# Kernel optimization log

Hardware: AMD Instinct MI355X
Metric: run time of the kernel (lower is better)

Reference implementation:

```python
import jax, jax.numpy as jnp
import numpy as np

D_MODEL = 1024
NUM_HEADS = 16
HEAD_DIM = D_MODEL // NUM_HEADS


def setup_inputs() -> dict:
    key = jax.random.key(0)
    ks = jax.random.split(key, 6)
    B, S = 2, 2048
    s = 1.0 / np.sqrt(D_MODEL)
    return {
        "x": jax.random.normal(ks[0], (B, S, D_MODEL), dtype=jnp.float32),
        "Wq": jax.random.normal(ks[1], (D_MODEL, D_MODEL), dtype=jnp.float32) * s,
        "Wk": jax.random.normal(ks[2], (D_MODEL, D_MODEL), dtype=jnp.float32) * s,
        "Wv": jax.random.normal(ks[3], (D_MODEL, D_MODEL), dtype=jnp.float32) * s,
        "Wo": jax.random.normal(ks[4], (D_MODEL, D_MODEL), dtype=jnp.float32) * s,
        "bo": jax.random.normal(ks[5], (D_MODEL,), dtype=jnp.float32) * 0.01,
    }


def reference(x, Wq, Wk, Wv, Wo, bo):
    b, n, _ = x.shape
    # QKV projections (no bias, qkv_bias=False); weights applied as x @ W^T like nn.Linear
    q = (x @ Wq.T).reshape(b, n, NUM_HEADS, HEAD_DIM).transpose(0, 2, 1, 3)  # [b,h,n,d]
    k = (x @ Wk.T).reshape(b, n, NUM_HEADS, HEAD_DIM).transpose(0, 2, 1, 3)
    v = (x @ Wv.T).reshape(b, n, NUM_HEADS, HEAD_DIM).transpose(0, 2, 1, 3)
    scores = jnp.einsum("bhqd,bhkd->bhqk", q, k)
    causal = jnp.tril(jnp.ones((n, n), dtype=bool))  # keep where True
    scores = jnp.where(causal, scores, -jnp.inf)
    weights = jax.nn.softmax(scores / np.sqrt(HEAD_DIM), axis=-1)
    # dropout p=0.0 -> identity (eval semantics)
    ctx = jnp.einsum("bhqk,bhkd->bhqd", weights, v)
    ctx = ctx.transpose(0, 2, 1, 3).reshape(b, n, D_MODEL)
    return ctx @ Wo.T + bo
```

## Files before the change

kernel.cpp:

```cpp
#include <hip/hip_runtime.h>

#define D_MODEL 1024
#define NUM_HEADS 16
#define HEAD_DIM 64
#define BATCH 2
#define SEQ 2048
#define MTOT (BATCH * SEQ)

typedef __attribute__((ext_vector_type(8))) short bf16x8;
typedef __attribute__((ext_vector_type(4))) short s16x4;
typedef __attribute__((ext_vector_type(4))) float f32x4;
typedef unsigned short u16;
typedef unsigned long long u64;

__device__ __forceinline__ u16 f2bf(float f) {
    unsigned u = __float_as_uint(f);
    return (u16)((u + 0x7FFFu + ((u >> 16) & 1u)) >> 16);
}
__device__ __forceinline__ float bf2f(u16 v) {
    return __uint_as_float((unsigned)v << 16);
}

__device__ __forceinline__ unsigned cvt_pk_bf16(float lo, float hi) {
    unsigned r;
    asm volatile("v_cvt_pk_bf16_f32 %0, %1, %2" : "=v"(r) : "v"(lo), "v"(hi));
    return r;
}

#if __has_builtin(__builtin_amdgcn_exp2f)
#define EXP2(x) __builtin_amdgcn_exp2f(x)
#else
#define EXP2(x) exp2f(x)
#endif

#define GLOAD16(gp, lp) __builtin_amdgcn_global_load_lds(                      \
    (const __attribute__((address_space(1))) void*)(gp),                       \
    (__attribute__((address_space(3))) void*)(lp), 16, 0, 0)

__global__ __launch_bounds__(256)
void cast_all_kernel(const float* __restrict__ x,  const float* __restrict__ Wq,
                     const float* __restrict__ Wk, const float* __restrict__ Wv,
                     const float* __restrict__ Wo, u16* __restrict__ dst)
{
    const int i = blockIdx.x * 256 + threadIdx.x;
    const float* src;
    int j;
    if (i < 524288) { src = x; j = i; }
    else if (i < 917504) {
        const int k = i - 524288;
        const int z = k >> 17;
        src = (z == 0) ? Wq : (z == 1) ? Wk : Wv;
        j = k & 0x1FFFF;
    } else { src = Wo; j = i - 917504; }
    const float4* s = reinterpret_cast<const float4*>(src) + (size_t)j * 2;
    float4 a = s[0], b = s[1];
    u16 tmp[8] = {f2bf(a.x), f2bf(a.y), f2bf(a.z), f2bf(a.w),
                  f2bf(b.x), f2bf(b.y), f2bf(b.z), f2bf(b.w)};
    *reinterpret_cast<int4*>(dst + (size_t)i * 8) = *reinterpret_cast<int4*>(tmp);
}

__global__ __launch_bounds__(256)
void gemm_qkv_kernel(const u16* __restrict__ A, const u16* __restrict__ B,
                     u16* __restrict__ Qo, u16* __restrict__ Ko, u16* __restrict__ Vt)
{
    __shared__ u16 Al[128 * 64];
    __shared__ u16 Bl[128 * 64];

    const int tid = threadIdx.x;
    const int l = tid & 63;
    const int w = tid >> 6;
    const int wm = w >> 1, wn = w & 1;
    const int lr = l & 15, lg = l >> 4;
    const int m0 = blockIdx.y * 128;
    const int n0 = blockIdx.x * 128;

    const int srow = tid >> 3;
    const int scol = ((tid & 7) ^ (srow & 7)) * 8;
    const int sxa = (lr & 7) * 8;

    f32x4 acc[4][4];
    #pragma unroll
    for (int i = 0; i < 4; ++i)
        #pragma unroll
        for (int j = 0; j < 4; ++j) acc[i][j] = (f32x4){0.f, 0.f, 0.f, 0.f};

    for (int k0 = 0; k0 < D_MODEL; k0 += 64) {
        __syncthreads();
        #pragma unroll
        for (int i = 0; i < 4; ++i) {
            const u16* ga = A + (size_t)(m0 + i * 32 + srow) * D_MODEL + k0 + scol;
            const u16* gb = B + (size_t)(n0 + i * 32 + srow) * D_MODEL + k0 + scol;
            GLOAD16(ga, Al + i * 2048 + w * 512);
            GLOAD16(gb, Bl + i * 2048 + w * 512);
        }
        __syncthreads();
        #pragma unroll
        for (int kc = 0; kc < 2; ++kc) {
            bf16x8 af[4], bfr[4];
            #pragma unroll
            for (int i = 0; i < 4; ++i)
                af[i] = *reinterpret_cast<const bf16x8*>(
                    &Al[(wm * 64 + i * 16 + lr) * 64 + ((kc * 32 + lg * 8) ^ sxa)]);
            #pragma unroll
            for (int j = 0; j < 4; ++j)
                bfr[j] = *reinterpret_cast<const bf16x8*>(
                    &Bl[(wn * 64 + j * 16 + lr) * 64 + ((kc * 32 + lg * 8) ^ sxa)]);
            #pragma unroll
            for (int i = 0; i < 4; ++i)
                #pragma unroll
                for (int j = 0; j < 4; ++j)
                    acc[i][j] = __builtin_amdgcn_mfma_f32_16x16x32_bf16(
                        af[i], bfr[j], acc[i][j], 0, 0, 0);
        }
    }

    const int z = (n0 >> 10);
    if (z < 2) {
        #pragma unroll
        for (int i = 0; i < 4; ++i) {
            #pragma unroll
            for (int r = 0; r < 4; ++r) {
                const int m = m0 + wm * 64 + i * 16 + lg * 4 + r;
                const int bb = m >> 11, s = m & (SEQ - 1);
                #pragma unroll
                for (int j = 0; j < 4; ++j) {
                    const int c = n0 + wn * 64 + j * 16 + lr;
                    const int cc = c & 1023, h = cc >> 6, d = cc & 63;
                    const size_t idx = ((size_t)(bb * NUM_HEADS + h) * SEQ + s) * 64 + d;
                    if (z == 0) Qo[idx] = f2bf(acc[i][j][r] * 0.18033688f);
                    else        Ko[idx] = f2bf(acc[i][j][r]);
                }
            }
        }
    } else {
        #pragma unroll
        for (int i = 0; i < 4; ++i) {
            const int mbase = m0 + wm * 64 + i * 16 + lg * 4;
            const int bb = mbase >> 11, s = mbase & (SEQ - 1);
            #pragma unroll
            for (int j = 0; j < 4; ++j) {
                const int c = n0 + wn * 64 + j * 16 + lr;
                const int cc = c & 1023, h = cc >> 6, d = cc & 63;
                u16 t4[4];
                #pragma unroll
                for (int r = 0; r < 4; ++r) t4[r] = f2bf(acc[i][j][r]);
                *reinterpret_cast<u64*>(
                    &Vt[((size_t)(bb * NUM_HEADS + h) * 64 + d) * SEQ + s]) =
                    *reinterpret_cast<u64*>(t4);
            }
        }
    }
}

__global__ __launch_bounds__(256)
void gemm_out_kernel(const u16* __restrict__ A, const u16* __restrict__ B,
                     const float* __restrict__ bias, float* __restrict__ out)
{
    __shared__ u16 Al[128 * 64];
    __shared__ u16 Bl[128 * 64];

    const int tid = threadIdx.x;
    const int l = tid & 63;
    const int w = tid >> 6;
    const int wm = w >> 1, wn = w & 1;
    const int lr = l & 15, lg = l >> 4;
    const int m0 = blockIdx.y * 128;
    const int n0 = blockIdx.x * 128;

    const int srow = tid >> 3;
    const int scol = ((tid & 7) ^ (srow & 7)) * 8;
    const int sxa = (lr & 7) * 8;

    f32x4 acc[4][4];
    #pragma unroll
    for (int i = 0; i < 4; ++i)
        #pragma unroll
        for (int j = 0; j < 4; ++j) acc[i][j] = (f32x4){0.f, 0.f, 0.f, 0.f};

    for (int k0 = 0; k0 < D_MODEL; k0 += 64) {
        __syncthreads();
        #pragma unroll
        for (int i = 0; i < 4; ++i) {
            const u16* ga = A + (size_t)(m0 + i * 32 + srow) * D_MODEL + k0 + scol;
            const u16* gb = B + (size_t)(n0 + i * 32 + srow) * D_MODEL + k0 + scol;
            GLOAD16(ga, Al + i * 2048 + w * 512);
            GLOAD16(gb, Bl + i * 2048 + w * 512);
        }
        __syncthreads();
        #pragma unroll
        for (int kc = 0; kc < 2; ++kc) {
            bf16x8 af[4], bfr[4];
            #pragma unroll
            for (int i = 0; i < 4; ++i)
                af[i] = *reinterpret_cast<const bf16x8*>(
                    &Al[(wm * 64 + i * 16 + lr) * 64 + ((kc * 32 + lg * 8) ^ sxa)]);
            #pragma unroll
            for (int j = 0; j < 4; ++j)
                bfr[j] = *reinterpret_cast<const bf16x8*>(
                    &Bl[(wn * 64 + j * 16 + lr) * 64 + ((kc * 32 + lg * 8) ^ sxa)]);
            #pragma unroll
            for (int i = 0; i < 4; ++i)
                #pragma unroll
                for (int j = 0; j < 4; ++j)
                    acc[i][j] = __builtin_amdgcn_mfma_f32_16x16x32_bf16(
                        af[i], bfr[j], acc[i][j], 0, 0, 0);
        }
    }

    #pragma unroll
    for (int i = 0; i < 4; ++i) {
        #pragma unroll
        for (int r = 0; r < 4; ++r) {
            const int m = m0 + wm * 64 + i * 16 + lg * 4 + r;
            #pragma unroll
            for (int j = 0; j < 4; ++j) {
                const int c = n0 + wn * 64 + j * 16 + lr;
                out[(size_t)m * D_MODEL + c] = acc[i][j][r] + bias[c];
            }
        }
    }
}

__device__ __forceinline__ void map_pair(int p, int& qt, int& ch) {
    if (p < 32)      { qt = 31 - (p >> 2); ch = p & 3; }
    else if (p < 56) { int t = p - 32; qt = 23 - t / 3; ch = t % 3; }
    else if (p < 72) { int t = p - 56; qt = 15 - (t >> 1); ch = t & 1; }
    else             { qt = 79 - p; ch = 0; }
}

__global__ __launch_bounds__(256)
void attn_kernel(const u16* __restrict__ Q, const u16* __restrict__ K,
                 const u16* __restrict__ Vt, u16* __restrict__ ctx,
                 u16* __restrict__ Opart, float* __restrict__ Lpart)
{
    __shared__ char LdsB[2][16384];

    const int tid = threadIdx.x;
    const int l = tid & 63;
    const int w = tid >> 6;
    const int lr = l & 15;
    const int lg = l >> 4;

    const int xcd  = blockIdx.x & 7;
    const int slot = blockIdx.x >> 3;
    const int bh   = xcd * 4 + slot / 80;
    int qt, ch;
    map_pair(slot % 80, qt, ch);

    const int ntiles = qt + 1;
    const int nch  = (qt + 8) >> 3;
    const int base = ntiles / nch, rem = ntiles % nch;
    const int start = ch * base + (ch < rem ? ch : rem);
    const int cnt   = base + (ch < rem ? 1 : 0);

    const size_t hbase = (size_t)bh * SEQ * 64;
    const int b = bh >> 4, h = bh & (NUM_HEADS - 1);
    const u16* __restrict__ Kh = K + hbase;
    const u16* __restrict__ Vh = Vt + hbase;

    const int q0 = qt * 64;
    const int qrow = q0 + w * 16 + lr;

    const int r0 = tid >> 3;
    const int c0 = ((tid & 7) ^ (r0 & 7)) * 8;
    const int r1 = (256 + tid) >> 3;
    const int c1 = ((tid & 7) ^ (r1 & 7)) * 8;
    const int d0b = tid * 16;
    const int d1b = 4096 + tid * 16;
    const int rswz = (lr & 7) << 4;

    bf16x8 qf0, qf1;
    {
        const u16* qp = Q + hbase + (size_t)qrow * 64 + lg * 8;
        qf0 = *reinterpret_cast<const bf16x8*>(qp);
        qf1 = *reinterpret_cast<const bf16x8*>(qp + 32);
    }

    f32x4 oacc[4];
    #pragma unroll
    for (int nb = 0; nb < 4; ++nb) oacc[nb] = (f32x4){0.f, 0.f, 0.f, 0.f};
    float lsum = 0.f;

    {
        char* kb = LdsB[0];
        char* vb = LdsB[0] + 8192;
        const int kb64 = start * 64;
        GLOAD16(Kh + (size_t)(kb64 + r0) * 64 + c0, kb + d0b);
        GLOAD16(Kh + (size_t)(kb64 + r1) * 64 + c1, kb + d1b);
        GLOAD16(Vh + (size_t)r0 * SEQ + kb64 + c0, vb + d0b);
        GLOAD16(Vh + (size_t)r1 * SEQ + kb64 + c1, vb + d1b);
    }

    for (int it = 0; it < cnt; ++it) {
        const int tile = start + it;
        const int buf = it & 1;
        if (it < cnt - 1) {
            const int kb64 = (tile + 1) * 64;
            char* kbl = LdsB[buf ^ 1];
            char* vbl = kbl + 8192;
            GLOAD16(Kh + (size_t)(kb64 + r0) * 64 + c0, kbl + d0b);
            GLOAD16(Kh + (size_t)(kb64 + r1) * 64 + c1, kbl + d1b);
            GLOAD16(Vh + (size_t)r0 * SEQ + kb64 + c0, vbl + d0b);
            GLOAD16(Vh + (size_t)r1 * SEQ + kb64 + c1, vbl + d1b);
            asm volatile("s_waitcnt vmcnt(4)" ::: "memory");
        } else {
            asm volatile("s_waitcnt vmcnt(0)" ::: "memory");
        }
        __builtin_amdgcn_s_barrier();

        const char* kbuf = LdsB[buf];
        const char* vbuf = kbuf + 8192;

        f32x4 s[4];
        __builtin_amdgcn_s_setprio(1);
        #pragma unroll
        for (int m = 0; m < 4; ++m) {
            s[m] = (f32x4){0.f, 0.f, 0.f, 0.f};
            const char* krow = kbuf + (16 * m + lr) * 128;
            bf16x8 kf0 = *reinterpret_cast<const bf16x8*>(krow + ((lg * 16) ^ rswz));
            bf16x8 kf1 = *reinterpret_cast<const bf16x8*>(krow + ((64 + lg * 16) ^ rswz));
            s[m] = __builtin_amdgcn_mfma_f32_16x16x32_bf16(kf0, qf0, s[m], 0, 0, 0);
            s[m] = __builtin_amdgcn_mfma_f32_16x16x32_bf16(kf1, qf1, s[m], 0, 0, 0);
        }
        __builtin_amdgcn_s_setprio(0);

        if (tile == qt) {
            #pragma unroll
            for (int m = 0; m < 4; ++m)
                #pragma unroll
                for (int r = 0; r < 4; ++r)
                    if (16 * m + 4 * lg + r > 16 * w + lr) s[m][r] = -1.0e38f;
        }

        float p[4][4];
        #pragma unroll
        for (int m = 0; m < 4; ++m)
            #pragma unroll
            for (int r = 0; r < 4; ++r) p[m][r] = EXP2(s[m][r]);

        {
            float a0 = (p[0][0] + p[0][1]) + (p[0][2] + p[0][3]);
            float a1 = (p[1][0] + p[1][1]) + (p[1][2] + p[1][3]);
            float a2 = (p[2][0] + p[2][1]) + (p[2][2] + p[2][3]);
            float a3 = (p[3][0] + p[3][1]) + (p[3][2] + p[3][3]);
            lsum += (a0 + a1) + (a2 + a3);
        }

        unsigned dw[4][2];
        #pragma unroll
        for (int m = 0; m < 4; ++m) {
            dw[m][0] = cvt_pk_bf16(p[m][0], p[m][1]);
            dw[m][1] = cvt_pk_bf16(p[m][2], p[m][3]);
        }

        __builtin_amdgcn_s_setprio(1);
        #pragma unroll
        for (int c = 0; c < 2; ++c) {
            union { unsigned u[4]; bf16x8 v; } pb;
            pb.u[0] = dw[2 * c][0];     pb.u[1] = dw[2 * c][1];
            pb.u[2] = dw[2 * c + 1][0]; pb.u[3] = dw[2 * c + 1][1];
            #pragma unroll
            for (int nb = 0; nb < 4; ++nb) {
                const char* vrow = vbuf + (16 * nb + lr) * 128;
                union { s16x4 hv[2]; bf16x8 v; } vf;
                vf.hv[0] = *reinterpret_cast<const s16x4*>(
                    vrow + ((c * 64 + lg * 8) ^ rswz));
                vf.hv[1] = *reinterpret_cast<const s16x4*>(
                    vrow + ((c * 64 + 32 + lg * 8) ^ rswz));
                oacc[nb] = __builtin_amdgcn_mfma_f32_16x16x32_bf16(
                    vf.v, pb.v, oacc[nb], 0, 0, 0);
            }
        }
        __builtin_amdgcn_s_setprio(0);

        __builtin_amdgcn_s_barrier();
    }

    lsum += __shfl_xor(lsum, 16);
    lsum += __shfl_xor(lsum, 32);

    if (nch == 1) {
        const float inv = 1.0f / lsum;
        u16* op = ctx + ((size_t)(b * SEQ) + qrow) * D_MODEL + h * 64 + 4 * lg;
        #pragma unroll
        for (int nb = 0; nb < 4; ++nb) {
            u16 t4[4];
            #pragma unroll
            for (int r = 0; r < 4; ++r) t4[r] = f2bf(oacc[nb][r] * inv);
            *reinterpret_cast<u64*>(op + 16 * nb) = *reinterpret_cast<u64*>(t4);
        }
    } else {
        const int slot4 = ((bh * 24 + (qt - 8)) << 2) + ch;
        u16* op = Opart + (size_t)slot4 * 4096 + (w * 16 + lr) * 64 + 4 * lg;
        #pragma unroll
        for (int nb = 0; nb < 4; ++nb) {
            u16 t4[4];
            #pragma unroll
            for (int r = 0; r < 4; ++r) t4[r] = f2bf(oacc[nb][r]);
            *reinterpret_cast<u64*>(op + 16 * nb) = *reinterpret_cast<u64*>(t4);
        }
        if (lg == 0) Lpart[slot4 * 64 + w * 16 + lr] = lsum;
    }
}

__global__ __launch_bounds__(64)
void attn_reduce_kernel(const u16* __restrict__ Opart,
                        const float* __restrict__ Lpart,
                        u16* __restrict__ ctx)
{
    const int blk = blockIdx.x;
    const int bh = blk / 24, qt8 = blk % 24;
    const int qt = qt8 + 8;
    const int nch = (qt + 8) >> 3;
    const int t = threadIdx.x;
    const int b = bh >> 4, h = bh & (NUM_HEADS - 1);
    const int slot0 = (bh * 24 + qt8) << 2;

    float acc[64] = {};
    float lt = 0.f;
    for (int ch = 0; ch < nch; ++ch) {
        const u16* op = Opart + (size_t)(slot0 + ch) * 4096 + t * 64;
        lt += Lpart[(slot0 + ch) * 64 + t];
        #pragma unroll
        for (int cchunk = 0; cchunk < 8; ++cchunk) {
            u16 v[8];
            *reinterpret_cast<int4*>(v) =
                *reinterpret_cast<const int4*>(op + cchunk * 8);
            #pragma unroll
            for (int j = 0; j < 8; ++j) acc[cchunk * 8 + j] += bf2f(v[j]);
        }
    }
    const float inv = 1.0f / lt;
    u16* orow = ctx + ((size_t)(b * SEQ) + qt * 64 + t) * D_MODEL + h * 64;
    #pragma unroll
    for (int cchunk = 0; cchunk < 8; ++cchunk) {
        u16 v[8];
        #pragma unroll
        for (int j = 0; j < 8; ++j) v[j] = f2bf(acc[cchunk * 8 + j] * inv);
        *reinterpret_cast<int4*>(orow + cchunk * 8) = *reinterpret_cast<int4*>(v);
    }
}


extern "C" void kernel_launch(void* const* d_in, const int* in_sizes, int n_in,
                              void* d_out, int out_size, void* d_ws, size_t ws_size,
                              hipStream_t stream)
{
    const float* x  = (const float*)d_in[0];
    const float* Wq = (const float*)d_in[1];
    const float* Wk = (const float*)d_in[2];
    const float* Wv = (const float*)d_in[3];
    const float* Wo = (const float*)d_in[4];
    const float* bo = (const float*)d_in[5];
    float* out = (float*)d_out;

    u16* xb   = (u16*)d_ws;
    u16* wqkv = xb   + (size_t)MTOT * D_MODEL;
    u16* wob  = wqkv + (size_t)3 * D_MODEL * D_MODEL;
    u16* Qw   = wob  + (size_t)D_MODEL * D_MODEL;
    u16* Kw   = Qw   + (size_t)MTOT * D_MODEL;
    u16* Vtw  = Kw   + (size_t)MTOT * D_MODEL;
    u16* ctxb = Vtw  + (size_t)MTOT * D_MODEL;
    u16* Opart = ctxb + (size_t)MTOT * D_MODEL;
    float* Lpart = (float*)(Opart + (size_t)3072 * 4096);

    cast_all_kernel<<<4096, 256, 0, stream>>>(x, Wq, Wk, Wv, Wo, xb);

    dim3 gq(3 * D_MODEL / 128, MTOT / 128);
    gemm_qkv_kernel<<<gq, 256, 0, stream>>>(xb, wqkv, Qw, Kw, Vtw);

    attn_kernel<<<dim3(2560), 256, 0, stream>>>(Qw, Kw, Vtw, ctxb, Opart, Lpart);
    attn_reduce_kernel<<<dim3(768), 64, 0, stream>>>(Opart, Lpart, ctxb);

    dim3 go(D_MODEL / 128, MTOT / 128);
    gemm_out_kernel<<<go, 256, 0, stream>>>(ctxb, wob, bo, out);
}
```

Baseline: 121.6 us.

## Rewrite QKV GEMM as 256x256 tile with software-pipelined LDS loads

Replaces the 128x128 QKV projection GEMM with a 512-thread, 256x256-tile kernel. Global-to-LDS loads for the next K step are interleaved with MFMA work on quarter-tiles, using explicit barriers, vmcnt waits and setprio. A swizzled block index improves L2 reuse. The aim is to raise arithmetic intensity and hide memory latency in the projection. The cost is much higher register and LDS pressure, and the fragile hand-written waitcnt ordering could race if the counts are wrong.

```diff
diff --git a/kernel.cpp b/kernel.cpp
--- a/kernel.cpp
+++ b/kernel.cpp
@@ -59,68 +59,165 @@
     *reinterpret_cast<int4*>(dst + (size_t)i * 8) = *reinterpret_cast<int4*>(tmp);
 }
 
-__global__ __launch_bounds__(256)
-void gemm_qkv_kernel(const u16* __restrict__ A, const u16* __restrict__ B,
-                     u16* __restrict__ Qo, u16* __restrict__ Ko, u16* __restrict__ Vt)
+__global__ __launch_bounds__(512, 2)
+void gemm_qkv256_kernel(const u16* __restrict__ A, const u16* __restrict__ B,
+                        u16* __restrict__ Qo, u16* __restrict__ Ko,
+                        u16* __restrict__ Vt)
 {
-    __shared__ u16 Al[128 * 64];
-    __shared__ u16 Bl[128 * 64];
+    __shared__ u16 Al[256 * 64];
+    __shared__ u16 Bl[256 * 64];
 
     const int tid = threadIdx.x;
     const int l = tid & 63;
     const int w = tid >> 6;
-    const int wm = w >> 1, wn = w & 1;
+    const int wm = w >> 2, wn = w & 3;
     const int lr = l & 15, lg = l >> 4;
-    const int m0 = blockIdx.y * 128;
-    const int n0 = blockIdx.x * 128;
+
+    const int bid = blockIdx.x;
+    const int swz = (bid & 7) * 24 + (bid >> 3);
+    const int mb = swz / 12, nb = swz % 12;
+    const int m0 = mb * 256, n0 = nb * 256;
 
     const int srow = tid >> 3;
     const int scol = ((tid & 7) ^ (srow & 7)) * 8;
-    const int sxa = (lr & 7) * 8;
-
-    f32x4 acc[4][4];
+    const int sxa  = (lr & 7) * 8;
+    const int dofs = tid * 8;
+
+    f32x4 acc[8][4];
     #pragma unroll
-    for (int i = 0; i < 4; ++i)
+    for (int i = 0; i < 8; ++i)
         #pragma unroll
         for (int j = 0; j < 4; ++j) acc[i][j] = (f32x4){0.f, 0.f, 0.f, 0.f};
 
-    for (int k0 = 0; k0 < D_MODEL; k0 += 64) {
-        __syncthreads();
-        #pragma unroll
-        for (int i = 0; i < 4; ++i) {
-            const u16* ga = A + (size_t)(m0 + i * 32 + srow) * D_MODEL + k0 + scol;
-            const u16* gb = B + (size_t)(n0 + i * 32 + srow) * D_MODEL + k0 + scol;
-            GLOAD16(ga, Al + i * 2048 + w * 512);
-            GLOAD16(gb, Bl + i * 2048 + w * 512);
-        }
-        __syncthreads();
-        #pragma unroll
-        for (int kc = 0; kc < 2; ++kc) {
-            bf16x8 af[4], bfr[4];
-            #pragma unroll
-            for (int i = 0; i < 4; ++i)
-                af[i] = *reinterpret_cast<const bf16x8*>(
-                    &Al[(wm * 64 + i * 16 + lr) * 64 + ((kc * 32 + lg * 8) ^ sxa)]);
-            #pragma unroll
-            for (int j = 0; j < 4; ++j)
-                bfr[j] = *reinterpret_cast<const bf16x8*>(
+    #pragma unroll
+    for (int q = 0; q < 4; ++q)
+        GLOAD16(B + (size_t)(n0 + q * 64 + srow) * D_MODEL + scol,
+                Bl + q * 4096 + dofs);
+    GLOAD16(A + (size_t)(m0 + 64  + srow) * D_MODEL + scol, Al + 4096  + dofs);
+    GLOAD16(A + (size_t)(m0 + 192 + srow) * D_MODEL + scol, Al + 12288 + dofs);
+
+    bf16x8 bfr[4][2];
+
+    for (int kt = 0; kt < 16; ++kt) {
+        const int k0 = kt * 64;
+        const int kn = k0 + 64;
+
+        __builtin_amdgcn_s_barrier();
+        GLOAD16(A + (size_t)(m0 + 0   + srow) * D_MODEL + k0 + scol, Al + 0    + dofs);
+        GLOAD16(A + (size_t)(m0 + 128 + srow) * D_MODEL + k0 + scol, Al + 8192 + dofs);
+        asm volatile("s_waitcnt vmcnt(2)" ::: "memory");
+        __builtin_amdgcn_s_barrier();
+        #pragma unroll
+        for (int j = 0; j < 4; ++j)
+            #pragma unroll
+            for (int kc = 0; kc < 2; ++kc)
+                bfr[j][kc] = *reinterpret_cast<const bf16x8*>(
                     &Bl[(wn * 64 + j * 16 + lr) * 64 + ((kc * 32 + lg * 8) ^ sxa)]);
-            #pragma unroll
-            for (int i = 0; i < 4; ++i)
+        {
+            bf16x8 af[2][2];
+            #pragma unroll
+            for (int i2 = 0; i2 < 2; ++i2)
+                #pragma unroll
+                for (int kc = 0; kc < 2; ++kc)
+                    af[i2][kc] = *reinterpret_cast<const bf16x8*>(
+                        &Al[(wm * 128 + (4 + i2) * 16 + lr) * 64 + ((kc * 32 + lg * 8) ^ sxa)]);
+            __builtin_amdgcn_s_setprio(1);
+            #pragma unroll
+            for (int i2 = 0; i2 < 2; ++i2)
                 #pragma unroll
                 for (int j = 0; j < 4; ++j)
-                    acc[i][j] = __builtin_amdgcn_mfma_f32_16x16x32_bf16(
-                        af[i], bfr[j], acc[i][j], 0, 0, 0);
+                    #pragma unroll
+                    for (int kc = 0; kc < 2; ++kc)
+                        acc[4 + i2][j] = __builtin_amdgcn_mfma_f32_16x16x32_bf16(
+                            af[i2][kc], bfr[j][kc], acc[4 + i2][j], 0, 0, 0);
+            __builtin_amdgcn_s_setprio(0);
+        }
+
+        __builtin_amdgcn_s_barrier();
+        if (kt < 15) {
+            #pragma unroll
+            for (int q = 0; q < 4; ++q)
+                GLOAD16(B + (size_t)(n0 + q * 64 + srow) * D_MODEL + kn + scol,
+                        Bl + q * 4096 + dofs);
+        }
+        {
+            bf16x8 af[2][2];
+            #pragma unroll
+            for (int i2 = 0; i2 < 2; ++i2)
+                #pragma unroll
+                for (int kc = 0; kc < 2; ++kc)
+                    af[i2][kc] = *reinterpret_cast<const bf16x8*>(
+                        &Al[(wm * 128 + (6 + i2) * 16 + lr) * 64 + ((kc * 32 + lg * 8) ^ sxa)]);
+            __builtin_amdgcn_s_setprio(1);
+            #pragma unroll
+            for (int i2 = 0; i2 < 2; ++i2)
+                #pragma unroll
+                for (int j = 0; j < 4; ++j)
+                    #pragma unroll
+                    for (int kc = 0; kc < 2; ++kc)
+                        acc[6 + i2][j] = __builtin_amdgcn_mfma_f32_16x16x32_bf16(
+                            af[i2][kc], bfr[j][kc], acc[6 + i2][j], 0, 0, 0);
+            __builtin_amdgcn_s_setprio(0);
+        }
+
+        __builtin_amdgcn_s_barrier();
+        if (kt < 15) {
+            GLOAD16(A + (size_t)(m0 + 64  + srow) * D_MODEL + kn + scol, Al + 4096  + dofs);
+            GLOAD16(A + (size_t)(m0 + 192 + srow) * D_MODEL + kn + scol, Al + 12288 + dofs);
+            asm volatile("s_waitcnt vmcnt(6)" ::: "memory");
+        } else {
+            asm volatile("s_waitcnt vmcnt(0)" ::: "memory");
+        }
+        __builtin_amdgcn_s_barrier();
+        {
+            bf16x8 af[2][2];
+            #pragma unroll
+            for (int i2 = 0; i2 < 2; ++i2)
+                #pragma unroll
+                for (int kc = 0; kc < 2; ++kc)
+                    af[i2][kc] = *reinterpret_cast<const bf16x8*>(
+                        &Al[(wm * 128 + i2 * 16 + lr) * 64 + ((kc * 32 + lg * 8) ^ sxa)]);
+            __builtin_amdgcn_s_setprio(1);
+            #pragma unroll
+            for (int i2 = 0; i2 < 2; ++i2)
+                #pragma unroll
+                for (int j = 0; j < 4; ++j)
+                    #pragma unroll
+                    for (int kc = 0; kc < 2; ++kc)
+                        acc[i2][j] = __builtin_amdgcn_mfma_f32_16x16x32_bf16(
+                            af[i2][kc], bfr[j][kc], acc[i2][j], 0, 0, 0);
+            __builtin_amdgcn_s_setprio(0);
+        }
+
+        __builtin_amdgcn_s_barrier();
+        {
+            bf16x8 af[2][2];
+            #pragma unroll
+            for (int i2 = 0; i2 < 2; ++i2)
+                #pragma unroll
+                for (int kc = 0; kc < 2; ++kc)
+                    af[i2][kc] = *reinterpret_cast<const bf16x8*>(
+                        &Al[(wm * 128 + (2 + i2) * 16 + lr) * 64 + ((kc * 32 + lg * 8) ^ sxa)]);
+            __builtin_amdgcn_s_setprio(1);
+            #pragma unroll
+            for (int i2 = 0; i2 < 2; ++i2)
+                #pragma unroll
+                for (int j = 0; j < 4; ++j)
+                    #pragma unroll
+                    for (int kc = 0; kc < 2; ++kc)
+                        acc[2 + i2][j] = __builtin_amdgcn_mfma_f32_16x16x32_bf16(
+                            af[i2][kc], bfr[j][kc], acc[2 + i2][j], 0, 0, 0);
+            __builtin_amdgcn_s_setprio(0);
         }
     }
 
     const int z = (n0 >> 10);
     if (z < 2) {
         #pragma unroll
-        for (int i = 0; i < 4; ++i) {
+        for (int i = 0; i < 8; ++i) {
             #pragma unroll
             for (int r = 0; r < 4; ++r) {
-                const int m = m0 + wm * 64 + i * 16 + lg * 4 + r;
+                const int m = m0 + wm * 128 + i * 16 + lg * 4 + r;
                 const int bb = m >> 11, s = m & (SEQ - 1);
                 #pragma unroll
                 for (int j = 0; j < 4; ++j) {
@@ -134,8 +231,8 @@
         }
     } else {
         #pragma unroll
-        for (int i = 0; i < 4; ++i) {
-            const int mbase = m0 + wm * 64 + i * 16 + lg * 4;
+        for (int i = 0; i < 8; ++i) {
+            const int mbase = m0 + wm * 128 + i * 16 + lg * 4;
             const int bb = mbase >> 11, s = mbase & (SEQ - 1);
             #pragma unroll
             for (int j = 0; j < 4; ++j) {
@@ -466,8 +563,7 @@
 
     cast_all_kernel<<<4096, 256, 0, stream>>>(x, Wq, Wk, Wv, Wo, xb);
 
-    dim3 gq(3 * D_MODEL / 128, MTOT / 128);
-    gemm_qkv_kernel<<<gq, 256, 0, stream>>>(xb, wqkv, Qw, Kw, Vtw);
+    gemm_qkv256_kernel<<<dim3(192), 512, 0, stream>>>(xb, wqkv, Qw, Kw, Vtw);
 
     attn_kernel<<<dim3(2560), 256, 0, stream>>>(Qw, Kw, Vtw, ctxb, Opart, Lpart);
     attn_reduce_kernel<<<dim3(768), 64, 0, stream>>>(Opart, Lpart, ctxb);
```

Measured after the change: 127.5 us. 1.05x slower.

## Split key tile across waves instead of queries, reduce partial outputs via LDS

Applied to the files above, without the earlier changes.

Each wave now owns 16 keys of every key tile and computes scores for all 64 queries, holding four Q fragments in registers. Per tile it loads only its own K rows and a quarter of the V slice from LDS, instead of every wave reading the whole K/V tile. The cost is a cross-wave reduction of partial outputs and row sums through LDS at the end, which adds several barriers. The PV MFMAs also run with half-zeroed operands, so that step issues twice as many MFMA instructions. The kernel needs 64 float accumulators per thread, which raises register pressure.

```diff
diff --git a/kernel.cpp b/kernel.cpp
--- a/kernel.cpp
+++ b/kernel.cpp
@@ -257,9 +257,7 @@
     const int b = bh >> 4, h = bh & (NUM_HEADS - 1);
     const u16* __restrict__ Kh = K + hbase;
     const u16* __restrict__ Vh = Vt + hbase;
-
     const int q0 = qt * 64;
-    const int qrow = q0 + w * 16 + lr;
 
     const int r0 = tid >> 3;
     const int c0 = ((tid & 7) ^ (r0 & 7)) * 8;
@@ -269,17 +267,21 @@
     const int d1b = 4096 + tid * 16;
     const int rswz = (lr & 7) << 4;
 
-    bf16x8 qf0, qf1;
-    {
-        const u16* qp = Q + hbase + (size_t)qrow * 64 + lg * 8;
-        qf0 = *reinterpret_cast<const bf16x8*>(qp);
-        qf1 = *reinterpret_cast<const bf16x8*>(qp + 32);
-    }
-
-    f32x4 oacc[4];
-    #pragma unroll
-    for (int nb = 0; nb < 4; ++nb) oacc[nb] = (f32x4){0.f, 0.f, 0.f, 0.f};
-    float lsum = 0.f;
+    bf16x8 qf[4][2];
+    #pragma unroll
+    for (int fq = 0; fq < 4; ++fq) {
+        const u16* qp = Q + hbase + (size_t)(q0 + fq * 16 + lr) * 64 + lg * 8;
+        qf[fq][0] = *reinterpret_cast<const bf16x8*>(qp);
+        qf[fq][1] = *reinterpret_cast<const bf16x8*>(qp + 32);
+    }
+    asm volatile("s_waitcnt vmcnt(0)" ::: "memory");
+
+    f32x4 acc[4][4];
+    #pragma unroll
+    for (int nb = 0; nb < 4; ++nb)
+        #pragma unroll
+        for (int fq = 0; fq < 4; ++fq) acc[nb][fq] = (f32x4){0.f, 0.f, 0.f, 0.f};
+    float lsumv[4] = {0.f, 0.f, 0.f, 0.f};
 
     {
         char* kb = LdsB[0];
@@ -311,82 +313,110 @@
         const char* kbuf = LdsB[buf];
         const char* vbuf = kbuf + 8192;
 
+        const char* krow = kbuf + (w * 16 + lr) * 128;
+        const bf16x8 kf0 = *reinterpret_cast<const bf16x8*>(krow + ((lg * 16) ^ rswz));
+        const bf16x8 kf1 = *reinterpret_cast<const bf16x8*>(krow + ((64 + lg * 16) ^ rswz));
+
+        union Vu { s16x4 hv[2]; bf16x8 v; } vf[4];
+        #pragma unroll
+        for (int nb = 0; nb < 4; ++nb) {
+            const char* vrow = vbuf + (16 * nb + lr) * 128;
+            vf[nb].hv[0] = *reinterpret_cast<const s16x4*>(
+                vrow + ((w * 32 + lg * 8) ^ rswz));
+            vf[nb].hv[1] = (s16x4){0, 0, 0, 0};
+        }
+
         f32x4 s[4];
         __builtin_amdgcn_s_setprio(1);
         #pragma unroll
-        for (int m = 0; m < 4; ++m) {
-            s[m] = (f32x4){0.f, 0.f, 0.f, 0.f};
-            const char* krow = kbuf + (16 * m + lr) * 128;
-            bf16x8 kf0 = *reinterpret_cast<const bf16x8*>(krow + ((lg * 16) ^ rswz));
-            bf16x8 kf1 = *reinterpret_cast<const bf16x8*>(krow + ((64 + lg * 16) ^ rswz));
-            s[m] = __builtin_amdgcn_mfma_f32_16x16x32_bf16(kf0, qf0, s[m], 0, 0, 0);
-            s[m] = __builtin_amdgcn_mfma_f32_16x16x32_bf16(kf1, qf1, s[m], 0, 0, 0);
+        for (int fq = 0; fq < 4; ++fq) {
+            s[fq] = (f32x4){0.f, 0.f, 0.f, 0.f};
+            s[fq] = __builtin_amdgcn_mfma_f32_16x16x32_bf16(kf0, qf[fq][0], s[fq], 0, 0, 0);
+            s[fq] = __builtin_amdgcn_mfma_f32_16x16x32_bf16(kf1, qf[fq][1], s[fq], 0, 0, 0);
         }
         __builtin_amdgcn_s_setprio(0);
 
         if (tile == qt) {
             #pragma unroll
-            for (int m = 0; m < 4; ++m)
+            for (int fq = 0; fq < 4; ++fq)
                 #pragma unroll
                 for (int r = 0; r < 4; ++r)
-                    if (16 * m + 4 * lg + r > 16 * w + lr) s[m][r] = -1.0e38f;
+                    if (w * 16 + 4 * lg + r > fq * 16 + lr) s[fq][r] = -1.0e38f;
         }
 
         float p[4][4];
         #pragma unroll
-        for (int m = 0; m < 4; ++m)
-            #pragma unroll
-            for (int r = 0; r < 4; ++r) p[m][r] = EXP2(s[m][r]);
-
-        {
-            float a0 = (p[0][0] + p[0][1]) + (p[0][2] + p[0][3]);
-            float a1 = (p[1][0] + p[1][1]) + (p[1][2] + p[1][3]);
-            float a2 = (p[2][0] + p[2][1]) + (p[2][2] + p[2][3]);
-            float a3 = (p[3][0] + p[3][1]) + (p[3][2] + p[3][3]);
-            lsum += (a0 + a1) + (a2 + a3);
-        }
-
-        unsigned dw[4][2];
-        #pragma unroll
-        for (int m = 0; m < 4; ++m) {
-            dw[m][0] = cvt_pk_bf16(p[m][0], p[m][1]);
-            dw[m][1] = cvt_pk_bf16(p[m][2], p[m][3]);
-        }
-
+        for (int fq = 0; fq < 4; ++fq) {
+            #pragma unroll
+            for (int r = 0; r < 4; ++r) p[fq][r] = EXP2(s[fq][r]);
+            lsumv[fq] += (p[fq][0] + p[fq][1]) + (p[fq][2] + p[fq][3]);
+        }
+
+        union Pu { unsigned u[4]; bf16x8 v; } pb[4];
+        #pragma unroll
+        for (int fq = 0; fq < 4; ++fq) {
+            pb[fq].u[0] = cvt_pk_bf16(p[fq][0], p[fq][1]);
+            pb[fq].u[1] = cvt_pk_bf16(p[fq][2], p[fq][3]);
+            pb[fq].u[2] = 0;
+            pb[fq].u[3] = 0;
+        }
         __builtin_amdgcn_s_setprio(1);
         #pragma unroll
-        for (int c = 0; c < 2; ++c) {
-            union { unsigned u[4]; bf16x8 v; } pb;
-            pb.u[0] = dw[2 * c][0];     pb.u[1] = dw[2 * c][1];
-            pb.u[2] = dw[2 * c + 1][0]; pb.u[3] = dw[2 * c + 1][1];
-            #pragma unroll
-            for (int nb = 0; nb < 4; ++nb) {
-                const char* vrow = vbuf + (16 * nb + lr) * 128;
-                union { s16x4 hv[2]; bf16x8 v; } vf;
-                vf.hv[0] = *reinterpret_cast<const s16x4*>(
-                    vrow + ((c * 64 + lg * 8) ^ rswz));
-                vf.hv[1] = *reinterpret_cast<const s16x4*>(
-                    vrow + ((c * 64 + 32 + lg * 8) ^ rswz));
-                oacc[nb] = __builtin_amdgcn_mfma_f32_16x16x32_bf16(
-                    vf.v, pb.v, oacc[nb], 0, 0, 0);
-            }
-        }
+        for (int nb = 0; nb < 4; ++nb)
+            #pragma unroll
+            for (int fq = 0; fq < 4; ++fq)
+                acc[nb][fq] = __builtin_amdgcn_mfma_f32_16x16x32_bf16(
+                    vf[nb].v, pb[fq].v, acc[nb][fq], 0, 0, 0);
         __builtin_amdgcn_s_setprio(0);
 
         __builtin_amdgcn_s_barrier();
     }
 
-    lsum += __shfl_xor(lsum, 16);
-    lsum += __shfl_xor(lsum, 32);
-
+    #pragma unroll
+    for (int fq = 0; fq < 4; ++fq) {
+        lsumv[fq] += __shfl_xor(lsumv[fq], 16);
+        lsumv[fq] += __shfl_xor(lsumv[fq], 32);
+    }
+    float* Lx = reinterpret_cast<float*>(&LdsB[0][0]);
+    if (lg == 0) {
+        #pragma unroll
+        for (int fq = 0; fq < 4; ++fq) Lx[(fq * 4 + w) * 16 + lr] = lsumv[fq];
+    }
+    __syncthreads();
+    const float lt = Lx[(w * 4 + 0) * 16 + lr] + Lx[(w * 4 + 1) * 16 + lr] +
+                     Lx[(w * 4 + 2) * 16 + lr] + Lx[(w * 4 + 3) * 16 + lr];
+    __syncthreads();
+
+    f32x4 fin[4];
+    f32x4* S = reinterpret_cast<f32x4*>(&LdsB[0][0]);
+    #pragma unroll
+    for (int hb = 0; hb < 2; ++hb) {
+        #pragma unroll
+        for (int fq = 0; fq < 4; ++fq)
+            #pragma unroll
+            for (int nbl = 0; nbl < 2; ++nbl)
+                S[(((fq * 4 + w) * 2 + nbl) * 64) + l] = acc[hb * 2 + nbl][fq];
+        __syncthreads();
+        #pragma unroll
+        for (int nbl = 0; nbl < 2; ++nbl) {
+            f32x4 t = S[(((w * 4 + 0) * 2 + nbl) * 64) + l];
+            t += S[(((w * 4 + 1) * 2 + nbl) * 64) + l];
+            t += S[(((w * 4 + 2) * 2 + nbl) * 64) + l];
+            t += S[(((w * 4 + 3) * 2 + nbl) * 64) + l];
+            fin[hb * 2 + nbl] = t;
+        }
+        __syncthreads();
+    }
+
+    const int qrow = q0 + w * 16 + lr;
     if (nch == 1) {
-        const float inv = 1.0f / lsum;
+        const float inv = 1.0f / lt;
         u16* op = ctx + ((size_t)(b * SEQ) + qrow) * D_MODEL + h * 64 + 4 * lg;
         #pragma unroll
         for (int nb = 0; nb < 4; ++nb) {
             u16 t4[4];
             #pragma unroll
-            for (int r = 0; r < 4; ++r) t4[r] = f2bf(oacc[nb][r] * inv);
+            for (int r = 0; r < 4; ++r) t4[r] = f2bf(fin[nb][r] * inv);
             *reinterpret_cast<u64*>(op + 16 * nb) = *reinterpret_cast<u64*>(t4);
         }
     } else {
@@ -396,10 +426,10 @@
         for (int nb = 0; nb < 4; ++nb) {
             u16 t4[4];
             #pragma unroll
-            for (int r = 0; r < 4; ++r) t4[r] = f2bf(oacc[nb][r]);
+            for (int r = 0; r < 4; ++r) t4[r] = f2bf(fin[nb][r]);
             *reinterpret_cast<u64*>(op + 16 * nb) = *reinterpret_cast<u64*>(t4);
         }
-        if (lg == 0) Lpart[slot4 * 64 + w * 16 + lr] = lsum;
+        if (lg == 0) Lpart[slot4 * 64 + w * 16 + lr] = lt;
     }
 }
 
```

Result: slower. 136.0 us (+11.8%).

## Process 128 query rows per attention block to reuse K/V tiles across two fragments

Applied to the files above, without the earlier changes.

Each attention workgroup now handles two 64-row query fragments (128 queries), so each K/V tile loaded into LDS and each K fragment read into registers feeds twice as many MFMAs. The grid halves and the split-KV chunk mapping, partial-output layout and reduce kernel are reworked for 128-row tiles. The aim is less global/LDS traffic and barrier overhead per unit of work, at the cost of more registers (double accumulators) and fewer, coarser blocks. This may lower occupancy or load balance on the causal triangle.

```diff
diff --git a/kernel.cpp b/kernel.cpp
--- a/kernel.cpp
+++ b/kernel.cpp
@@ -221,11 +221,11 @@
     }
 }
 
-__device__ __forceinline__ void map_pair(int p, int& qt, int& ch) {
-    if (p < 32)      { qt = 31 - (p >> 2); ch = p & 3; }
-    else if (p < 56) { int t = p - 32; qt = 23 - t / 3; ch = t % 3; }
-    else if (p < 72) { int t = p - 56; qt = 15 - (t >> 1); ch = t & 1; }
-    else             { qt = 79 - p; ch = 0; }
+__device__ __forceinline__ void map_pair128(int p, int& qt2, int& ch) {
+    if (p < 16)      { qt2 = 15 - (p >> 2); ch = p & 3; }
+    else if (p < 28) { int t = p - 16; qt2 = 11 - t / 3; ch = t % 3; }
+    else if (p < 36) { int t = p - 28; qt2 = 7 - (t >> 1); ch = t & 1; }
+    else             { qt2 = 39 - p; ch = 0; }
 }
 
 __global__ __launch_bounds__(256)
@@ -243,12 +243,12 @@
 
     const int xcd  = blockIdx.x & 7;
     const int slot = blockIdx.x >> 3;
-    const int bh   = xcd * 4 + slot / 80;
-    int qt, ch;
-    map_pair(slot % 80, qt, ch);
-
-    const int ntiles = qt + 1;
-    const int nch  = (qt + 8) >> 3;
+    const int bh   = xcd * 4 + slot / 40;
+    int qt2, ch;
+    map_pair128(slot % 40, qt2, ch);
+
+    const int ntiles = 2 * qt2 + 2;
+    const int nch  = (ntiles + 7) >> 3;
     const int base = ntiles / nch, rem = ntiles % nch;
     const int start = ch * base + (ch < rem ? ch : rem);
     const int cnt   = base + (ch < rem ? 1 : 0);
@@ -257,9 +257,7 @@
     const int b = bh >> 4, h = bh & (NUM_HEADS - 1);
     const u16* __restrict__ Kh = K + hbase;
     const u16* __restrict__ Vh = Vt + hbase;
-
-    const int q0 = qt * 64;
-    const int qrow = q0 + w * 16 + lr;
+    const int q0 = qt2 * 128;
 
     const int r0 = tid >> 3;
     const int c0 = ((tid & 7) ^ (r0 & 7)) * 8;
@@ -269,17 +267,21 @@
     const int d1b = 4096 + tid * 16;
     const int rswz = (lr & 7) << 4;
 
-    bf16x8 qf0, qf1;
-    {
-        const u16* qp = Q + hbase + (size_t)qrow * 64 + lg * 8;
-        qf0 = *reinterpret_cast<const bf16x8*>(qp);
-        qf1 = *reinterpret_cast<const bf16x8*>(qp + 32);
-    }
-
-    f32x4 oacc[4];
-    #pragma unroll
-    for (int nb = 0; nb < 4; ++nb) oacc[nb] = (f32x4){0.f, 0.f, 0.f, 0.f};
-    float lsum = 0.f;
+    bf16x8 qf[2][2];
+    #pragma unroll
+    for (int fq = 0; fq < 2; ++fq) {
+        const u16* qp = Q + hbase + (size_t)(q0 + fq * 64 + w * 16 + lr) * 64 + lg * 8;
+        qf[fq][0] = *reinterpret_cast<const bf16x8*>(qp);
+        qf[fq][1] = *reinterpret_cast<const bf16x8*>(qp + 32);
+    }
+    asm volatile("s_waitcnt vmcnt(0)" ::: "memory");
+
+    f32x4 acc[2][4];
+    #pragma unroll
+    for (int fq = 0; fq < 2; ++fq)
+        #pragma unroll
+        for (int nb = 0; nb < 4; ++nb) acc[fq][nb] = (f32x4){0.f, 0.f, 0.f, 0.f};
+    float lsumv[2] = {0.f, 0.f};
 
     {
         char* kb = LdsB[0];
@@ -311,64 +313,67 @@
         const char* kbuf = LdsB[buf];
         const char* vbuf = kbuf + 8192;
 
-        f32x4 s[4];
+        bf16x8 kf[4][2];
+        #pragma unroll
+        for (int m = 0; m < 4; ++m) {
+            const char* krow = kbuf + (16 * m + lr) * 128;
+            kf[m][0] = *reinterpret_cast<const bf16x8*>(krow + ((lg * 16) ^ rswz));
+            kf[m][1] = *reinterpret_cast<const bf16x8*>(krow + ((64 + lg * 16) ^ rswz));
+        }
+
+        const bool diag = (tile >= 2 * qt2);
+        const int koff0 = (tile - 2 * qt2) * 64;
+
+        unsigned dw[2][4][2];
         __builtin_amdgcn_s_setprio(1);
         #pragma unroll
-        for (int m = 0; m < 4; ++m) {
-            s[m] = (f32x4){0.f, 0.f, 0.f, 0.f};
-            const char* krow = kbuf + (16 * m + lr) * 128;
-            bf16x8 kf0 = *reinterpret_cast<const bf16x8*>(krow + ((lg * 16) ^ rswz));
-            bf16x8 kf1 = *reinterpret_cast<const bf16x8*>(krow + ((64 + lg * 16) ^ rswz));
-            s[m] = __builtin_amdgcn_mfma_f32_16x16x32_bf16(kf0, qf0, s[m], 0, 0, 0);
-            s[m] = __builtin_amdgcn_mfma_f32_16x16x32_bf16(kf1, qf1, s[m], 0, 0, 0);
-        }
-        __builtin_amdgcn_s_setprio(0);
-
-        if (tile == qt) {
-            #pragma unroll
-            for (int m = 0; m < 4; ++m)
-                #pragma unroll
-                for (int r = 0; r < 4; ++r)
-                    if (16 * m + 4 * lg + r > 16 * w + lr) s[m][r] = -1.0e38f;
-        }
-
-        float p[4][4];
-        #pragma unroll
-        for (int m = 0; m < 4; ++m)
-            #pragma unroll
-            for (int r = 0; r < 4; ++r) p[m][r] = EXP2(s[m][r]);
-
-        {
-            float a0 = (p[0][0] + p[0][1]) + (p[0][2] + p[0][3]);
-            float a1 = (p[1][0] + p[1][1]) + (p[1][2] + p[1][3]);
-            float a2 = (p[2][0] + p[2][1]) + (p[2][2] + p[2][3]);
-            float a3 = (p[3][0] + p[3][1]) + (p[3][2] + p[3][3]);
-            lsum += (a0 + a1) + (a2 + a3);
-        }
-
-        unsigned dw[4][2];
-        #pragma unroll
-        for (int m = 0; m < 4; ++m) {
-            dw[m][0] = cvt_pk_bf16(p[m][0], p[m][1]);
-            dw[m][1] = cvt_pk_bf16(p[m][2], p[m][3]);
-        }
-
-        __builtin_amdgcn_s_setprio(1);
+        for (int fq = 0; fq < 2; ++fq) {
+            f32x4 s[4];
+            #pragma unroll
+            for (int m = 0; m < 4; ++m) {
+                s[m] = (f32x4){0.f, 0.f, 0.f, 0.f};
+                s[m] = __builtin_amdgcn_mfma_f32_16x16x32_bf16(kf[m][0], qf[fq][0], s[m], 0, 0, 0);
+                s[m] = __builtin_amdgcn_mfma_f32_16x16x32_bf16(kf[m][1], qf[fq][1], s[m], 0, 0, 0);
+            }
+            if (diag) {
+                const int qloc = fq * 64 + w * 16 + lr;
+                #pragma unroll
+                for (int m = 0; m < 4; ++m)
+                    #pragma unroll
+                    for (int r = 0; r < 4; ++r)
+                        if (koff0 + 16 * m + 4 * lg + r > qloc) s[m][r] = -1.0e38f;
+            }
+            float p[4][4];
+            #pragma unroll
+            for (int m = 0; m < 4; ++m) {
+                #pragma unroll
+                for (int r = 0; r < 4; ++r) p[m][r] = EXP2(s[m][r]);
+                lsumv[fq] += (p[m][0] + p[m][1]) + (p[m][2] + p[m][3]);
+                dw[fq][m][0] = cvt_pk_bf16(p[m][0], p[m][1]);
+                dw[fq][m][1] = cvt_pk_bf16(p[m][2], p[m][3]);
+            }
+        }
+
         #pragma unroll
         for (int c = 0; c < 2; ++c) {
-            union { unsigned u[4]; bf16x8 v; } pb;
-            pb.u[0] = dw[2 * c][0];     pb.u[1] = dw[2 * c][1];
-            pb.u[2] = dw[2 * c + 1][0]; pb.u[3] = dw[2 * c + 1][1];
+            union Pu { unsigned u[4]; bf16x8 v; } pb[2];
+            #pragma unroll
+            for (int fq = 0; fq < 2; ++fq) {
+                pb[fq].u[0] = dw[fq][2 * c][0];     pb[fq].u[1] = dw[fq][2 * c][1];
+                pb[fq].u[2] = dw[fq][2 * c + 1][0]; pb[fq].u[3] = dw[fq][2 * c + 1][1];
+            }
             #pragma unroll
             for (int nb = 0; nb < 4; ++nb) {
                 const char* vrow = vbuf + (16 * nb + lr) * 128;
-                union { s16x4 hv[2]; bf16x8 v; } vf;
+                union Vu { s16x4 hv[2]; bf16x8 v; } vf;
                 vf.hv[0] = *reinterpret_cast<const s16x4*>(
                     vrow + ((c * 64 + lg * 8) ^ rswz));
                 vf.hv[1] = *reinterpret_cast<const s16x4*>(
                     vrow + ((c * 64 + 32 + lg * 8) ^ rswz));
-                oacc[nb] = __builtin_amdgcn_mfma_f32_16x16x32_bf16(
-                    vf.v, pb.v, oacc[nb], 0, 0, 0);
+                acc[0][nb] = __builtin_amdgcn_mfma_f32_16x16x32_bf16(
+                    vf.v, pb[0].v, acc[0][nb], 0, 0, 0);
+                acc[1][nb] = __builtin_amdgcn_mfma_f32_16x16x32_bf16(
+                    vf.v, pb[1].v, acc[1][nb], 0, 0, 0);
             }
         }
         __builtin_amdgcn_s_setprio(0);
@@ -376,51 +381,62 @@
         __builtin_amdgcn_s_barrier();
     }
 
-    lsum += __shfl_xor(lsum, 16);
-    lsum += __shfl_xor(lsum, 32);
+    #pragma unroll
+    for (int fq = 0; fq < 2; ++fq) {
+        lsumv[fq] += __shfl_xor(lsumv[fq], 16);
+        lsumv[fq] += __shfl_xor(lsumv[fq], 32);
+    }
 
     if (nch == 1) {
-        const float inv = 1.0f / lsum;
-        u16* op = ctx + ((size_t)(b * SEQ) + qrow) * D_MODEL + h * 64 + 4 * lg;
-        #pragma unroll
-        for (int nb = 0; nb < 4; ++nb) {
-            u16 t4[4];
-            #pragma unroll
-            for (int r = 0; r < 4; ++r) t4[r] = f2bf(oacc[nb][r] * inv);
-            *reinterpret_cast<u64*>(op + 16 * nb) = *reinterpret_cast<u64*>(t4);
+        #pragma unroll
+        for (int fq = 0; fq < 2; ++fq) {
+            const float inv = 1.0f / lsumv[fq];
+            const int qrow = q0 + fq * 64 + w * 16 + lr;
+            u16* op = ctx + ((size_t)(b * SEQ) + qrow) * D_MODEL + h * 64 + 4 * lg;
+            #pragma unroll
+            for (int nb = 0; nb < 4; ++nb) {
+                u16 t4[4];
+                #pragma unroll
+                for (int r = 0; r < 4; ++r) t4[r] = f2bf(acc[fq][nb][r] * inv);
+                *reinterpret_cast<u64*>(op + 16 * nb) = *reinterpret_cast<u64*>(t4);
+            }
         }
     } else {
-        const int slot4 = ((bh * 24 + (qt - 8)) << 2) + ch;
-        u16* op = Opart + (size_t)slot4 * 4096 + (w * 16 + lr) * 64 + 4 * lg;
-        #pragma unroll
-        for (int nb = 0; nb < 4; ++nb) {
-            u16 t4[4];
-            #pragma unroll
-            for (int r = 0; r < 4; ++r) t4[r] = f2bf(oacc[nb][r]);
-            *reinterpret_cast<u64*>(op + 16 * nb) = *reinterpret_cast<u64*>(t4);
-        }
-        if (lg == 0) Lpart[slot4 * 64 + w * 16 + lr] = lsum;
-    }
-}
-
-__global__ __launch_bounds__(64)
+        const int slot4 = ((bh * 12 + (qt2 - 4)) << 2) + ch;
+        #pragma unroll
+        for (int fq = 0; fq < 2; ++fq) {
+            const int rloc = fq * 64 + w * 16 + lr;
+            u16* op = Opart + (size_t)slot4 * 8192 + rloc * 64 + 4 * lg;
+            #pragma unroll
+            for (int nb = 0; nb < 4; ++nb) {
+                u16 t4[4];
+                #pragma unroll
+                for (int r = 0; r < 4; ++r) t4[r] = f2bf(acc[fq][nb][r]);
+                *reinterpret_cast<u64*>(op + 16 * nb) = *reinterpret_cast<u64*>(t4);
+            }
+            if (lg == 0) Lpart[slot4 * 128 + rloc] = lsumv[fq];
+        }
+    }
+}
+
+__global__ __launch_bounds__(128)
 void attn_reduce_kernel(const u16* __restrict__ Opart,
                         const float* __restrict__ Lpart,
                         u16* __restrict__ ctx)
 {
     const int blk = blockIdx.x;
-    const int bh = blk / 24, qt8 = blk % 24;
-    const int qt = qt8 + 8;
-    const int nch = (qt + 8) >> 3;
+    const int bh = blk / 12, idx = blk % 12;
+    const int qt2 = idx + 4;
+    const int nch = (2 * qt2 + 2 + 7) >> 3;
     const int t = threadIdx.x;
     const int b = bh >> 4, h = bh & (NUM_HEADS - 1);
-    const int slot0 = (bh * 24 + qt8) << 2;
+    const int slot0 = (bh * 12 + idx) << 2;
 
     float acc[64] = {};
     float lt = 0.f;
     for (int ch = 0; ch < nch; ++ch) {
-        const u16* op = Opart + (size_t)(slot0 + ch) * 4096 + t * 64;
-        lt += Lpart[(slot0 + ch) * 64 + t];
+        const u16* op = Opart + (size_t)(slot0 + ch) * 8192 + t * 64;
+        lt += Lpart[(slot0 + ch) * 128 + t];
         #pragma unroll
         for (int cchunk = 0; cchunk < 8; ++cchunk) {
             u16 v[8];
@@ -431,7 +447,7 @@
         }
     }
     const float inv = 1.0f / lt;
-    u16* orow = ctx + ((size_t)(b * SEQ) + qt * 64 + t) * D_MODEL + h * 64;
+    u16* orow = ctx + ((size_t)(b * SEQ) + qt2 * 128 + t) * D_MODEL + h * 64;
     #pragma unroll
     for (int cchunk = 0; cchunk < 8; ++cchunk) {
         u16 v[8];
@@ -462,15 +478,15 @@
     u16* Vtw  = Kw   + (size_t)MTOT * D_MODEL;
     u16* ctxb = Vtw  + (size_t)MTOT * D_MODEL;
     u16* Opart = ctxb + (size_t)MTOT * D_MODEL;
-    float* Lpart = (float*)(Opart + (size_t)3072 * 4096);
+    float* Lpart = (float*)(Opart + (size_t)1536 * 8192);
 
     cast_all_kernel<<<4096, 256, 0, stream>>>(x, Wq, Wk, Wv, Wo, xb);
 
     dim3 gq(3 * D_MODEL / 128, MTOT / 128);
     gemm_qkv_kernel<<<gq, 256, 0, stream>>>(xb, wqkv, Qw, Kw, Vtw);
 
-    attn_kernel<<<dim3(2560), 256, 0, stream>>>(Qw, Kw, Vtw, ctxb, Opart, Lpart);
-    attn_reduce_kernel<<<dim3(768), 64, 0, stream>>>(Opart, Lpart, ctxb);
+    attn_kernel<<<dim3(1280), 256, 0, stream>>>(Qw, Kw, Vtw, ctxb, Opart, Lpart);
+    attn_reduce_kernel<<<dim3(384), 128, 0, stream>>>(Opart, Lpart, ctxb);
 
     dim3 go(D_MODEL / 128, MTOT / 128);
     gemm_out_kernel<<<go, 256, 0, stream>>>(ctxb, wob, bo, out);
```

Result: slower. 124.3 us (+2.2%).
